# Kernel optimization log

Measured on AMD Instinct MI355X. Metric: run time of the kernel, lower is better.

## Reference

```python
import jax, jax.numpy as jnp
import numpy as np

B, S, H = 4, 2048, 576
NH, NKV, HD = 9, 3, 64
NEG = -1e9


def rotate_half(x):
    x1, x2 = x[..., : HD // 2], x[..., HD // 2 :]
    return jnp.concatenate((-x2, x1), axis=-1)


def setup_inputs() -> dict:
    key = jax.random.key(0)
    ks = jax.random.split(key, 6)
    x = jax.random.normal(ks[0], (B, S, H), dtype=jnp.float32)
    # realistic RoPE tables
    inv_freq = 1.0 / (10000.0 ** (np.arange(0, HD, 2, dtype=np.float32) / HD))
    pos = np.arange(S, dtype=np.float32)
    freqs = np.outer(pos, inv_freq)            # [S, HD//2]
    emb = np.concatenate([freqs, freqs], -1)   # [S, HD]
    cos = jnp.asarray(np.cos(emb), dtype=jnp.float32)
    sin = jnp.asarray(np.sin(emb), dtype=jnp.float32)
    # causal additive mask [1,1,S,S]
    causal = jnp.tril(jnp.ones((S, S), dtype=jnp.bool_))
    mask = jnp.where(causal, 0.0, NEG).astype(jnp.float32)[None, None]
    sc = 1.0 / np.sqrt(H)
    Wq = jax.random.normal(ks[1], (H, NH * HD), dtype=jnp.float32) * sc
    Wk = jax.random.normal(ks[2], (H, NKV * HD), dtype=jnp.float32) * sc
    Wv = jax.random.normal(ks[3], (H, NKV * HD), dtype=jnp.float32) * sc
    Wo = jax.random.normal(ks[4], (NH * HD, H), dtype=jnp.float32) * sc
    return {"x": x, "cos": cos, "sin": sin, "mask": mask,
            "Wq": Wq, "Wk": Wk, "Wv": Wv, "Wo": Wo}


def reference(x, cos, sin, mask, Wq, Wk, Wv, Wo):
    b, s, _ = x.shape
    # projections -> [b, heads, s, hd]
    q = (x @ Wq).reshape(b, s, NH, HD).transpose(0, 2, 1, 3)
    k = (x @ Wk).reshape(b, s, NKV, HD).transpose(0, 2, 1, 3)
    v = (x @ Wv).reshape(b, s, NKV, HD).transpose(0, 2, 1, 3)
    c = cos[None, None]  # [1,1,s,hd]
    sn = sin[None, None]
    q = q * c + rotate_half(q) * sn
    k = k * c + rotate_half(k) * sn
    # GQA: repeat_interleave KV heads to match query heads
    groups = NH // NKV
    k = jnp.repeat(k, groups, axis=1)
    v = jnp.repeat(v, groups, axis=1)
    scores = jnp.einsum("bhqd,bhkd->bhqk", q, k) / np.sqrt(HD)
    scores = scores + mask
    probs = jax.nn.softmax(scores, axis=-1)
    out = jnp.einsum("bhqk,bhkd->bhqd", probs, v)
    out = out.transpose(0, 2, 1, 3).reshape(b, s, NH * HD)
    return out @ Wo
```

## Files before the change

### kernel.cpp

```cpp
#include <hip/hip_runtime.h>
#include <math.h>

typedef __attribute__((ext_vector_type(4))) float f32x4;
typedef __attribute__((ext_vector_type(8))) short short8;
typedef __attribute__((ext_vector_type(8))) __bf16 bf16x8;
typedef __attribute__((ext_vector_type(2))) __bf16 bf16x2;
typedef __attribute__((ext_vector_type(2))) unsigned uint32x2;

#define NB 4
#define NS 2048
#define NHID 576
#define NHEADS 9
#define NKVH 3
#define NHD 64
#define NM (NB * NS)
#define NQKV 960
#define QKS 768
#define NGRP 3
#define QSC 0.18033688f

static __device__ __forceinline__ unsigned short f2bf(float f) {
  union { float f; unsigned u; } v; v.f = f;
  unsigned r = v.u + 0x7FFFu + ((v.u >> 16) & 1u);
  return (unsigned short)(r >> 16);
}
static __device__ __forceinline__ unsigned pk2bf(float a, float b) {
  bf16x2 h;
  h.x = (__bf16)a;
  h.y = (__bf16)b;
  return __builtin_bit_cast(unsigned, h);
}
static __device__ __forceinline__ float bf2f(unsigned short h) {
  union { unsigned u; float f; } v; v.u = ((unsigned)h) << 16;
  return v.f;
}
static __device__ __forceinline__ f32x4 mfma16(short8 a, short8 b, f32x4 c) {
  return __builtin_amdgcn_mfma_f32_16x16x32_bf16(
      __builtin_bit_cast(bf16x8, a), __builtin_bit_cast(bf16x8, b), c, 0, 0, 0);
}
static __device__ __forceinline__ void gload16(const void* g, void* l) {
  __builtin_amdgcn_global_load_lds(
      (const __attribute__((address_space(1))) void*)g,
      (__attribute__((address_space(3))) void*)l, 16, 0, 0);
}

__global__ __launch_bounds__(256)
void k_cvt(const float* __restrict__ src, unsigned short* __restrict__ dst, const int n8) {
  const int t = blockIdx.x * 256 + threadIdx.x;
  if (t >= n8) return;
  const f32x4* sp = (const f32x4*)(src + (size_t)t * 8);
  f32x4 a = sp[0], b = sp[1];
  union { short8 v; unsigned short u[8]; } o;
#pragma unroll
  for (int e = 0; e < 4; ++e) { o.u[e] = f2bf(a[e]); o.u[4 + e] = f2bf(b[e]); }
  *(short8*)(dst + (size_t)t * 8) = o.v;
}

__global__ __launch_bounds__(256)
void k_transpose_cvt(const float* __restrict__ src, unsigned short* __restrict__ dst,
                     const int R, const int C) {
  __shared__ unsigned short tile[64 * 72];
  const int t = threadIdx.x;
  const int r0 = blockIdx.y * 64, c0 = blockIdx.x * 64;
  {
    const int rl = t >> 2, cb = (t & 3) * 16;
    const float* sp = src + (size_t)(r0 + rl) * C + c0 + cb;
#pragma unroll
    for (int jj = 0; jj < 4; ++jj) {
      f32x4 v = *(const f32x4*)(sp + jj * 4);
#pragma unroll
      for (int e = 0; e < 4; ++e) tile[rl * 72 + cb + jj * 4 + e] = f2bf(v[e]);
    }
  }
  __syncthreads();
  {
    const int cl = t >> 2, rb = (t & 3) * 16;
    union { short8 v; unsigned short u[8]; } o0, o1;
#pragma unroll
    for (int jj = 0; jj < 8; ++jj) {
      o0.u[jj] = tile[(rb + jj) * 72 + cl];
      o1.u[jj] = tile[(rb + 8 + jj) * 72 + cl];
    }
    unsigned short* dp = dst + (size_t)(c0 + cl) * R + r0 + rb;
    *(short8*)dp = o0.v;
    *(short8*)(dp + 8) = o1.v;
  }
}

template <int MODE>
__global__ __launch_bounds__(256)
void k_gemm_bt(const unsigned short* __restrict__ A,
               const unsigned short* __restrict__ Bt,
               void* __restrict__ Cv,
               unsigned short* __restrict__ vtb,
               const float* __restrict__ cosT,
               const float* __restrict__ sinT,
               const int M, const int N, const int K) {
  __shared__ unsigned short a_lds[2][128 * 64];
  __shared__ unsigned short b_lds[2][128 * 64];
  const int tid = threadIdx.x;
  const int w = tid >> 6, l = tid & 63, g = l >> 4, c = l & 15;
  const int tm = blockIdx.y * 128, tn = blockIdx.x * 128;
  const int wm = w >> 1, wn = w & 1;
  f32x4 acc[4][4] = {};
  const int nk = K >> 6;

#define GSTAGE(k0, half)                                                   \
  {                                                                        \
    _Pragma("unroll")                                                      \
    for (int q = 0; q < 4; ++q) {                                          \
      const int o = q * 4096 + w * 1024 + l * 16;                          \
      const int row = o >> 7;                                              \
      const int wb = (o & 127) ^ ((row & 7) << 4);                         \
      gload16(A + (size_t)(tm + row) * K + (k0) + (wb >> 1),               \
              (void*)(a_lds[half] + ((q * 4096 + w * 1024) >> 1)));        \
      gload16(Bt + (size_t)(tn + row) * K + (k0) + (wb >> 1),              \
              (void*)(b_lds[half] + ((q * 4096 + w * 1024) >> 1)));        \
    }                                                                      \
  }

  GSTAGE(0, 0);

  for (int k = 0; k < nk; ++k) {
    if (k + 1 < nk) {
      GSTAGE((k + 1) << 6, (k + 1) & 1);
      asm volatile("s_waitcnt vmcnt(8)" ::: "memory");
    } else {
      asm volatile("s_waitcnt vmcnt(0)" ::: "memory");
    }
    __builtin_amdgcn_s_barrier();
    __builtin_amdgcn_sched_barrier(0);
    const char* al = (const char*)a_lds[k & 1];
    const char* bl = (const char*)b_lds[k & 1];
#pragma unroll
    for (int dc = 0; dc < 2; ++dc) {
      short8 af[4], bf[4];
#pragma unroll
      for (int mt = 0; mt < 4; ++mt) {
        const int row = wm * 64 + mt * 16 + c;
        const int byt = ((row << 7) + (dc << 6) + (g << 4)) ^ ((row & 7) << 4);
        af[mt] = *(const short8*)(al + byt);
      }
#pragma unroll
      for (int nt = 0; nt < 4; ++nt) {
        const int row = wn * 64 + nt * 16 + c;
        const int byt = ((row << 7) + (dc << 6) + (g << 4)) ^ ((row & 7) << 4);
        bf[nt] = *(const short8*)(bl + byt);
      }
      __builtin_amdgcn_s_setprio(1);
#pragma unroll
      for (int mt = 0; mt < 4; ++mt)
#pragma unroll
        for (int nt = 0; nt < 4; ++nt)
          acc[mt][nt] = mfma16(af[mt], bf[nt], acc[mt][nt]);
      __builtin_amdgcn_s_setprio(0);
    }
    __builtin_amdgcn_sched_barrier(0);
    __builtin_amdgcn_s_barrier();
  }
#undef GSTAGE

  if (MODE == 1) {
#pragma unroll
    for (int mt = 0; mt < 4; ++mt)
#pragma unroll
      for (int nt = 0; nt < 4; ++nt) {
        const int cc = tn + wn * 64 + nt * 16 + c;
        if (cc < N) {
#pragma unroll
          for (int i = 0; i < 4; ++i) {
            const size_t rr = (size_t)(tm + wm * 64 + mt * 16 + 4 * g + i);
            ((float*)Cv)[rr * N + cc] = acc[mt][nt][i];
          }
        }
      }
  } else if (tn < 768) {
    const float qs = (tn + wn * 64) < 576 ? QSC : 1.0f;
    unsigned short* Cp = (unsigned short*)Cv;
#pragma unroll
    for (int mt = 0; mt < 4; ++mt)
#pragma unroll
      for (int i = 0; i < 4; ++i) {
        const int rr = tm + wm * 64 + mt * 16 + 4 * g + i;
        const int s = rr & (NS - 1);
        const float* cb = cosT + (size_t)s * NHD;
        const float* sb = sinT + (size_t)s * NHD;
#pragma unroll
        for (int p = 0; p < 2; ++p) {
          const float cn = cb[p * 16 + c];
          const float sn = sb[p * 16 + c];
          const float lo = acc[mt][p][i];
          const float hi = acc[mt][p + 2][i];
          const size_t base = (size_t)rr * QKS + tn + wn * 64 + p * 16 + c;
          Cp[base] = f2bf((lo * cn - hi * sn) * qs);
          Cp[base + 32] = f2bf((hi * cn + lo * sn) * qs);
        }
      }
  } else {
#pragma unroll
    for (int mt = 0; mt < 4; ++mt)
#pragma unroll
      for (int nt = 0; nt < 4; ++nt) {
        const int cc = tn + wn * 64 + nt * 16 + c;
        if (cc < 960) {
          const int rr0 = tm + wm * 64 + mt * 16 + 4 * g;
          const int bb = rr0 >> 11, ss = rr0 & (NS - 1);
          const int grp = bb * NKVH + ((cc - 768) >> 6);
          const int d = (cc - 768) & 63;
          uint32x2 pk;
          pk.x = pk2bf(acc[mt][nt][0], acc[mt][nt][1]);
          pk.y = pk2bf(acc[mt][nt][2], acc[mt][nt][3]);
          *(uint32x2*)(vtb + (size_t)grp * (NHD * NS) + (size_t)d * NS + ss) = pk;
        }
      }
  }
}

__global__ __launch_bounds__(256)
void k_attn(const unsigned short* __restrict__ qkv,
            const unsigned short* __restrict__ vt,
            unsigned short* __restrict__ ao) {
  __shared__ unsigned short kv_s[2][2][4096];
  __shared__ unsigned short p_s[4][1024];
  const int tid = threadIdx.x;
  const int w = tid >> 6, l = tid & 63, g = l >> 4, c = l & 15;
  const int bh = blockIdx.x;
  const int qt = 31 - (int)blockIdx.y;
  const int b = bh / NHEADS, h = bh - b * NHEADS, kh = h / NGRP;

  const int lr = l >> 3;
  const int swz = ((l & 7) ^ lr) << 4;
  const int r0 = 16 * w + lr;
  const int cs = (c & 7) << 4;

  const char* kp0 = (const char*)(qkv + (size_t)b * NS * QKS + NHEADS * NHD + kh * NHD) +
                    (size_t)r0 * (QKS * 2) + swz;
  const char* kp1 = kp0 + 8 * (QKS * 2);
  const char* vp0 = (const char*)(vt + (size_t)(b * NKVH + kh) * NHD * NS) +
                    (size_t)r0 * (NS * 2) + swz;
  const char* vp1 = vp0 + 8 * (NS * 2);

  const size_t qrow = (size_t)(b * NS + qt * 64 + w * 16 + c) * QKS + h * NHD;
  const short8 qf0 = *(const short8*)(qkv + qrow + g * 8);
  const short8 qf1 = *(const short8*)(qkv + qrow + 32 + g * 8);

  const short8 ones = {0x3F80, 0x3F80, 0x3F80, 0x3F80, 0x3F80, 0x3F80, 0x3F80, 0x3F80};

  f32x4 ot[4] = {};
  f32x4 lacc = {};
  float m = -1e30f;
  const int q_g = qt * 64 + w * 16 + c;

#define STAGE(BUF)                                                \
  {                                                               \
    gload16(kp0, kv_s[BUF][0] + 16 * w * 64);                     \
    gload16(kp1, kv_s[BUF][0] + (16 * w + 8) * 64);               \
    gload16(vp0, kv_s[BUF][1] + 16 * w * 64);                     \
    gload16(vp1, kv_s[BUF][1] + (16 * w + 8) * 64);               \
    kp0 += 64 * (QKS * 2); kp1 += 64 * (QKS * 2);                 \
    vp0 += 128; vp1 += 128;                                       \
  }

#define COMPUTE(BUF, jj)                                                        \
  {                                                                             \
    const char* kl = (const char*)kv_s[BUF][0];                                 \
    const char* vl = (const char*)kv_s[BUF][1];                                 \
    f32x4 st[4] = {};                                                           \
    _Pragma("unroll")                                                           \
    for (int dc = 0; dc < 2; ++dc) {                                            \
      const int col = (dc * 64 + g * 16) ^ cs;                                  \
      const short8 qf = dc ? qf1 : qf0;                                         \
      _Pragma("unroll")                                                         \
      for (int nt = 0; nt < 4; ++nt) {                                          \
        short8 kf = *(const short8*)(kl + (nt * 16 + c) * 128 + col);           \
        st[nt] = mfma16(kf, qf, st[nt]);                                        \
      }                                                                         \
    }                                                                           \
    if ((jj) == qt) {                                                           \
      _Pragma("unroll")                                                         \
      for (int nt = 0; nt < 4; ++nt)                                            \
        _Pragma("unroll")                                                       \
        for (int i = 0; i < 4; ++i) {                                           \
          const int kvg = (jj) * 64 + nt * 16 + 4 * g + i;                      \
          if (kvg > q_g) st[nt][i] = -1e30f;                                    \
        }                                                                       \
    }                                                                           \
    float m0 = fmaxf(fmaxf(st[0][0], st[0][1]), st[0][2]);                      \
    float m1 = fmaxf(fmaxf(st[0][3], st[1][0]), st[1][1]);                      \
    float m2 = fmaxf(fmaxf(st[1][2], st[1][3]), st[2][0]);                      \
    float m3 = fmaxf(fmaxf(st[2][1], st[2][2]), st[2][3]);                      \
    float m4 = fmaxf(fmaxf(st[3][0], st[3][1]), st[3][2]);                      \
    float pm = fmaxf(fmaxf(fmaxf(m0, m1), fmaxf(m2, m3)), fmaxf(m4, st[3][3]));\
    pm = fmaxf(pm, __shfl_xor(pm, 16));                                         \
    pm = fmaxf(pm, __shfl_xor(pm, 32));                                         \
    if (!__all(pm <= m + 8.0f)) {                                               \
      const float scl = exp2f(m - pm);                                          \
      m = pm;                                                                   \
      lacc *= scl;                                                              \
      _Pragma("unroll")                                                         \
      for (int nt = 0; nt < 4; ++nt) ot[nt] *= scl;                             \
    }                                                                           \
    {                                                                           \
      char* pw = (char*)p_s[w];                                                 \
      _Pragma("unroll")                                                         \
      for (int nt = 0; nt < 4; ++nt) {                                          \
        float p0 = exp2f(st[nt][0] - m);                                        \
        float p1 = exp2f(st[nt][1] - m);                                        \
        float p2 = exp2f(st[nt][2] - m);                                        \
        float p3 = exp2f(st[nt][3] - m);                                        \
        uint32x2 pk;                                                            \
        pk.x = pk2bf(p0, p1);                                                   \
        pk.y = pk2bf(p2, p3);                                                   \
        *(uint32x2*)(pw + c * 128 + ((nt * 32 + g * 8) ^ cs)) = pk;             \
      }                                                                         \
      _Pragma("unroll")                                                         \
      for (int dc = 0; dc < 2; ++dc) {                                          \
        const int col = (dc * 64 + g * 16) ^ cs;                                \
        short8 pf = *(const short8*)(pw + c * 128 + col);                       \
        lacc = mfma16(ones, pf, lacc);                                          \
        _Pragma("unroll")                                                       \
        for (int nt = 0; nt < 4; ++nt) {                                        \
          short8 vf = *(const short8*)(vl + (nt * 16 + c) * 128 + col);         \
          ot[nt] = mfma16(vf, pf, ot[nt]);                                      \
        }                                                                       \
      }                                                                         \
    }                                                                           \
  }

  STAGE(0);

  for (int j = 0; j <= qt; j += 2) {
    if (j < qt) {
      STAGE(1);
      asm volatile("s_waitcnt vmcnt(4)" ::: "memory");
    } else {
      asm volatile("s_waitcnt vmcnt(0)" ::: "memory");
    }
    __builtin_amdgcn_s_barrier();
    __builtin_amdgcn_sched_barrier(0);
    COMPUTE(0, j);
    __builtin_amdgcn_sched_barrier(0);
    __builtin_amdgcn_s_barrier();
    if (j + 1 > qt) break;
    if (j + 1 < qt) {
      STAGE(0);
      asm volatile("s_waitcnt vmcnt(4)" ::: "memory");
    } else {
      asm volatile("s_waitcnt vmcnt(0)" ::: "memory");
    }
    __builtin_amdgcn_s_barrier();
    __builtin_amdgcn_sched_barrier(0);
    COMPUTE(1, j + 1);
    __builtin_amdgcn_sched_barrier(0);
    __builtin_amdgcn_s_barrier();
  }
#undef STAGE
#undef COMPUTE

  {
    char* ol = (char*)kv_s[0][0];
    const float inv = __builtin_amdgcn_rcpf(lacc[0]);
#pragma unroll
    for (int nt = 0; nt < 4; ++nt) {
      uint32x2 pk;
      pk.x = pk2bf(ot[nt][0] * inv, ot[nt][1] * inv);
      pk.y = pk2bf(ot[nt][2] * inv, ot[nt][3] * inv);
      *(uint32x2*)(ol + (w * 16 + c) * 128 + ((nt * 32 + g * 8) ^ cs)) = pk;
    }
  }
  __syncthreads();
  {
    const char* ol = (const char*)kv_s[0][0];
    const int rr = tid >> 2, cb = tid & 3;
    const int rk = (rr & 7) << 4;
    short8 v0 = *(const short8*)(ol + rr * 128 + ((cb * 32) ^ rk));
    short8 v1 = *(const short8*)(ol + rr * 128 + ((cb * 32 + 16) ^ rk));
    char* aop = (char*)(ao + (size_t)(b * NS + qt * 64 + rr) * NHID + h * NHD + cb * 16);
    *(short8*)aop = v0;
    *(short8*)(aop + 16) = v1;
  }
}

extern "C" void kernel_launch(void* const* d_in, const int* in_sizes, int n_in,
                              void* d_out, int out_size, void* d_ws, size_t ws_size,
                              hipStream_t stream) {
  const float* x = (const float*)d_in[0];
  const float* cosT = (const float*)d_in[1];
  const float* sinT = (const float*)d_in[2];
  const float* Wq = (const float*)d_in[4];
  const float* Wk = (const float*)d_in[5];
  const float* Wv = (const float*)d_in[6];
  const float* Wo = (const float*)d_in[7];

  unsigned short* xb = (unsigned short*)d_ws;
  unsigned short* wqkvT = xb + (size_t)NM * NHID;
  unsigned short* woT = wqkvT + (size_t)NQKV * NHID;
  unsigned short* qkv = woT + (size_t)NHID * NHID;
  unsigned short* vt = qkv + (size_t)NM * QKS;
  unsigned short* ao = xb;

  k_cvt<<<dim3((NM * NHID / 8 + 255) / 256), 256, 0, stream>>>(x, xb, NM * NHID / 8);
  k_transpose_cvt<<<dim3(9, 9), 256, 0, stream>>>(Wq, wqkvT, NHID, NHID);
  k_transpose_cvt<<<dim3(3, 9), 256, 0, stream>>>(Wk, wqkvT + (size_t)576 * 576, NHID, 192);
  k_transpose_cvt<<<dim3(3, 9), 256, 0, stream>>>(Wv, wqkvT + (size_t)768 * 576, NHID, 192);
  k_transpose_cvt<<<dim3(9, 9), 256, 0, stream>>>(Wo, woT, NHID, NHID);
  k_gemm_bt<0><<<dim3((NQKV + 127) / 128, NM / 128), 256, 0, stream>>>(
      xb, wqkvT, (void*)qkv, vt, cosT, sinT, NM, NQKV, NHID);
  k_attn<<<dim3(NB * NHEADS, NS / 64), 256, 0, stream>>>(qkv, vt, ao);
  k_gemm_bt<1><<<dim3((NHID + 127) / 128, NM / 128), 256, 0, stream>>>(
      ao, woT, d_out, nullptr, nullptr, nullptr, NM, NHID, NHID);
}
```

Baseline: 103.4 us.

## Merge prep kernels into one launch and hoist V loads in attention

Folds the x bf16 conversion and the four weight transpose-convert launches into a single kernel that dispatches on block index, cutting four kernel launches. In attention, V fragments are loaded from LDS right after the QK MFMAs so their latency overlaps the softmax, at the cost of more live registers. The max-rescale check now compares each lane's own max first and runs the cross-lane shuffles only when a rescale is needed. The risk is register pressure lowering occupancy.

```diff
diff --git a/kernel.cpp b/kernel.cpp
--- a/kernel.cpp
+++ b/kernel.cpp
@@ -45,23 +45,33 @@
 }
 
 __global__ __launch_bounds__(256)
-void k_cvt(const float* __restrict__ src, unsigned short* __restrict__ dst, const int n8) {
-  const int t = blockIdx.x * 256 + threadIdx.x;
-  if (t >= n8) return;
-  const f32x4* sp = (const f32x4*)(src + (size_t)t * 8);
-  f32x4 a = sp[0], b = sp[1];
-  union { short8 v; unsigned short u[8]; } o;
-#pragma unroll
-  for (int e = 0; e < 4; ++e) { o.u[e] = f2bf(a[e]); o.u[4 + e] = f2bf(b[e]); }
-  *(short8*)(dst + (size_t)t * 8) = o.v;
-}
-
-__global__ __launch_bounds__(256)
-void k_transpose_cvt(const float* __restrict__ src, unsigned short* __restrict__ dst,
-                     const int R, const int C) {
+void k_prep(const float* __restrict__ x, unsigned short* __restrict__ xb,
+            const float* __restrict__ Wq, const float* __restrict__ Wk,
+            const float* __restrict__ Wv, const float* __restrict__ Wo,
+            unsigned short* __restrict__ wqkvT, unsigned short* __restrict__ woT) {
   __shared__ unsigned short tile[64 * 72];
+  int bid = blockIdx.x;
+  if (bid < 2304) {
+    const int t = bid * 256 + threadIdx.x;
+    const f32x4* sp = (const f32x4*)(x + (size_t)t * 8);
+    f32x4 a = sp[0], b = sp[1];
+    union { short8 v; unsigned short u[8]; } o;
+#pragma unroll
+    for (int e = 0; e < 4; ++e) { o.u[e] = f2bf(a[e]); o.u[4 + e] = f2bf(b[e]); }
+    *(short8*)(xb + (size_t)t * 8) = o.v;
+    return;
+  }
+  bid -= 2304;
+  const float* src;
+  unsigned short* dst;
+  int C, bx, by;
+  if (bid < 81) { src = Wq; dst = wqkvT; C = 576; bx = bid % 9; by = bid / 9; }
+  else if (bid < 108) { int b2 = bid - 81; src = Wk; dst = wqkvT + 576 * 576; C = 192; bx = b2 % 3; by = b2 / 3; }
+  else if (bid < 135) { int b2 = bid - 108; src = Wv; dst = wqkvT + 768 * 576; C = 192; bx = b2 % 3; by = b2 / 3; }
+  else { int b2 = bid - 135; src = Wo; dst = woT; C = 576; bx = b2 % 9; by = b2 / 9; }
+  const int R = 576;
   const int t = threadIdx.x;
-  const int r0 = blockIdx.y * 64, c0 = blockIdx.x * 64;
+  const int r0 = by * 64, c0 = bx * 64;
   {
     const int rl = t >> 2, cb = (t & 3) * 16;
     const float* sp = src + (size_t)(r0 + rl) * C + c0 + cb;
@@ -276,6 +286,14 @@
         st[nt] = mfma16(kf, qf, st[nt]);                                        \
       }                                                                         \
     }                                                                           \
+    short8 vf[8];                                                               \
+    _Pragma("unroll")                                                           \
+    for (int dc = 0; dc < 2; ++dc) {                                            \
+      const int col = (dc * 64 + g * 16) ^ cs;                                  \
+      _Pragma("unroll")                                                         \
+      for (int nt = 0; nt < 4; ++nt)                                            \
+        vf[dc * 4 + nt] = *(const short8*)(vl + (nt * 16 + c) * 128 + col);     \
+    }                                                                           \
     if ((jj) == qt) {                                                           \
       _Pragma("unroll")                                                         \
       for (int nt = 0; nt < 4; ++nt)                                            \
@@ -290,12 +308,14 @@
     float m2 = fmaxf(fmaxf(st[1][2], st[1][3]), st[2][0]);                      \
     float m3 = fmaxf(fmaxf(st[2][1], st[2][2]), st[2][3]);                      \
     float m4 = fmaxf(fmaxf(st[3][0], st[3][1]), st[3][2]);                      \
-    float pm = fmaxf(fmaxf(fmaxf(m0, m1), fmaxf(m2, m3)), fmaxf(m4, st[3][3]));\
-    pm = fmaxf(pm, __shfl_xor(pm, 16));                                         \
-    pm = fmaxf(pm, __shfl_xor(pm, 32));                                         \
-    if (!__all(pm <= m + 8.0f)) {                                               \
-      const float scl = exp2f(m - pm);                                          \
-      m = pm;                                                                   \
+    float inmax = fmaxf(fmaxf(fmaxf(m0, m1), fmaxf(m2, m3)),                    \
+                        fmaxf(m4, st[3][3]));                                   \
+    if (!__all(inmax <= m + 8.0f)) {                                            \
+      float pm = fmaxf(inmax, __shfl_xor(inmax, 16));                           \
+      pm = fmaxf(pm, __shfl_xor(pm, 32));                                       \
+      const float mn = fmaxf(m, pm);                                            \
+      const float scl = exp2f(m - mn);                                          \
+      m = mn;                                                                   \
       lacc *= scl;                                                              \
       _Pragma("unroll")                                                         \
       for (int nt = 0; nt < 4; ++nt) ot[nt] *= scl;                             \
@@ -319,10 +339,8 @@
         short8 pf = *(const short8*)(pw + c * 128 + col);                       \
         lacc = mfma16(ones, pf, lacc);                                          \
         _Pragma("unroll")                                                       \
-        for (int nt = 0; nt < 4; ++nt) {                                        \
-          short8 vf = *(const short8*)(vl + (nt * 16 + c) * 128 + col);         \
-          ot[nt] = mfma16(vf, pf, ot[nt]);                                      \
-        }                                                                       \
+        for (int nt = 0; nt < 4; ++nt)                                          \
+          ot[nt] = mfma16(vf[dc * 4 + nt], pf, ot[nt]);                         \
       }                                                                         \
     }                                                                           \
   }
@@ -399,11 +417,7 @@
   unsigned short* vt = qkv + (size_t)NM * QKS;
   unsigned short* ao = xb;
 
-  k_cvt<<<dim3((NM * NHID / 8 + 255) / 256), 256, 0, stream>>>(x, xb, NM * NHID / 8);
-  k_transpose_cvt<<<dim3(9, 9), 256, 0, stream>>>(Wq, wqkvT, NHID, NHID);
-  k_transpose_cvt<<<dim3(3, 9), 256, 0, stream>>>(Wk, wqkvT + (size_t)576 * 576, NHID, 192);
-  k_transpose_cvt<<<dim3(3, 9), 256, 0, stream>>>(Wv, wqkvT + (size_t)768 * 576, NHID, 192);
-  k_transpose_cvt<<<dim3(9, 9), 256, 0, stream>>>(Wo, woT, NHID, NHID);
+  k_prep<<<dim3(2304 + 216), 256, 0, stream>>>(x, xb, Wq, Wk, Wv, Wo, wqkvT, woT);
   k_gemm_bt<0><<<dim3((NQKV + 127) / 128, NM / 128), 256, 0, stream>>>(
       xb, wqkvT, (void*)qkv, vt, cosT, sinT, NM, NQKV, NHID);
   k_attn<<<dim3(NB * NHEADS, NS / 64), 256, 0, stream>>>(qkv, vt, ao);
```

After: 94.55 us. 8.5% less time.
